# Optimization experiments

Hardware: AMD Instinct MI355X
Metric: run time of the kernel (lower is better)

The kernel has to match this reference:

```python
import jax, jax.numpy as jnp
import numpy as np

B, N, C_IN = 8, 2048, 2


def _pdist(x):
    # (B,N,N) pairwise euclidean distances
    d2 = jnp.sum((x[:, :, None, :] - x[:, None, :, :]) ** 2, axis=-1)
    return jnp.sqrt(d2)


def _knn_idx(x, k):
    d = _pdist(x)
    return jnp.argsort(d, axis=-1)[:, :, :k]  # includes self (dist 0)


def _ball_idx(x, radius, nsample):
    # deterministic ball query: neighbors with dist<=radius in ascending index
    # order, cyclically repeated if fewer than nsample (self is always in ball)
    d = _pdist(x)
    n = x.shape[1]
    mask = d <= radius
    ar = jnp.arange(n)
    order = jnp.argsort(jnp.where(mask, ar, ar + n), axis=-1)  # valid idx first
    count = jnp.sum(mask, axis=-1, keepdims=True)               # >= 1
    pos = jnp.arange(nsample)[None, None, :] % count            # (B,N,nsample)
    return jnp.take_along_axis(order, pos, axis=-1)


def _gather(x, idx):
    # x: (B,N,C), idx: (B,N,S) -> (B,N,S,C)
    return jax.vmap(lambda pts, ind: pts[ind])(x, idx)


def _mlp2(f, w0, b0, w1, b1):
    # 1x1 Conv2D stack == per-neighbor dense + relu
    f = jnp.maximum(jnp.einsum('bnsc,cd->bnsd', f, w0) + b0, 0.0)
    f = jnp.maximum(jnp.einsum('bnsc,cd->bnsd', f, w1) + b1, 0.0)
    return f


def _dense_relu(x, w, b):
    return jnp.maximum(x @ w + b, 0.0)


def _forward(x,
             sa1_w0, sa1_b0, sa1_w1, sa1_b1,
             sa2_w0, sa2_b0, sa2_w1, sa2_b1,
             sa3_w0, sa3_b0, sa3_w1, sa3_b1,
             fp1_w0, fp1_b0, fp1_w1, fp1_b1,
             fp2_w0, fp2_b0, fp2_w1, fp2_b1,
             fc1_w, fc1_b, fc2_w, fc2_b, out_w, out_b):
    # SA1: knn(k=32) on raw points, mlps [64,64], mean over neighbors
    x1 = jnp.mean(_mlp2(_gather(x, _knn_idx(x, 32)), sa1_w0, sa1_b0, sa1_w1, sa1_b1), axis=2)
    # SA2: ball query radius=0.2, nsample=32, mlps [128,128]
    x2 = jnp.mean(_mlp2(_gather(x1, _ball_idx(x1, 0.2, 32)), sa2_w0, sa2_b0, sa2_w1, sa2_b1), axis=2)
    # SA3: ball query radius=0.4, nsample=64, mlps [256,256]
    x3 = jnp.mean(_mlp2(_gather(x2, _ball_idx(x2, 0.4, 64)), sa3_w0, sa3_b0, sa3_w1, sa3_b1), axis=2)
    # FP1: dense mlps on local (x2), concat global (x3)
    h = _dense_relu(_dense_relu(x2, fp1_w0, fp1_b0), fp1_w1, fp1_b1)
    h = jnp.concatenate([h, x3], axis=-1)
    # FP2: dense mlps on local (x1), concat previous
    g = _dense_relu(_dense_relu(x1, fp2_w0, fp2_b0), fp2_w1, fp2_b1)
    g = jnp.concatenate([g, h], axis=-1)
    g = _dense_relu(g, fc1_w, fc1_b)
    g = _dense_relu(g, fc2_w, fc2_b)
    return jax.nn.sigmoid(g @ out_w + out_b)  # (B,N,1)


def setup_inputs() -> dict:
    key = jax.random.key(0)
    ks = iter(jax.random.split(key, 40))
    def w(i, o):
        return (jax.random.normal(next(ks), (i, o), jnp.float32) / np.sqrt(i)).astype(jnp.float32)
    def b(o):
        return jnp.zeros((o,), jnp.float32)
    inp = {
        'x': jax.random.normal(next(ks), (B, N, C_IN), jnp.float32),
        'sa1_w0': w(2, 64),   'sa1_b0': b(64),  'sa1_w1': w(64, 64),   'sa1_b1': b(64),
        'sa2_w0': w(64, 128), 'sa2_b0': b(128), 'sa2_w1': w(128, 128), 'sa2_b1': b(128),
        'sa3_w0': w(128, 256),'sa3_b0': b(256), 'sa3_w1': w(256, 256), 'sa3_b1': b(256),
        'fp1_w0': w(128, 512),'fp1_b0': b(512), 'fp1_w1': w(512, 512), 'fp1_b1': b(512),
        'fp2_w0': w(64, 256), 'fp2_b0': b(256), 'fp2_w1': w(256, 256), 'fp2_b1': b(256),
        'fc1_w': w(1024, 256),'fc1_b': b(256),
        'fc2_w': w(256, 128), 'fc2_b': b(128),
        'out_w': w(128, 1),   'out_b': b(1),
    }
    return inp


def reference(x,
              sa1_w0, sa1_b0, sa1_w1, sa1_b1,
              sa2_w0, sa2_b0, sa2_w1, sa2_b1,
              sa3_w0, sa3_b0, sa3_w1, sa3_b1,
              fp1_w0, fp1_b0, fp1_w1, fp1_b1,
              fp2_w0, fp2_b0, fp2_w1, fp2_b1,
              fc1_w, fc1_b, fc2_w, fc2_b, out_w, out_b):
    return _forward(x,
                    sa1_w0, sa1_b0, sa1_w1, sa1_b1,
                    sa2_w0, sa2_b0, sa2_w1, sa2_b1,
                    sa3_w0, sa3_b0, sa3_w1, sa3_b1,
                    fp1_w0, fp1_b0, fp1_w1, fp1_b1,
                    fp2_w0, fp2_b0, fp2_w1, fp2_b1,
                    fc1_w, fc1_b, fc2_w, fc2_b, out_w, out_b)
```

## Files before the change

kernel.cpp:

```cpp
#include <hip/hip_runtime.h>
#include <hip/hip_bf16.h>
#include <cstdint>

#define M_ROWS 16384

typedef __attribute__((ext_vector_type(8))) short short8;
typedef __attribute__((ext_vector_type(4))) float f32x4;

__device__ __forceinline__ unsigned long long umin64(unsigned long long a,
                                                     unsigned long long b) {
  return a < b ? a : b;
}

struct TJobs {
  const float* W[8];
  __hip_bfloat16* Wt[8];
  int K[8], N[8], bx[8], off[8];
};

__global__ __launch_bounds__(256) void prologue_kernel(
    TJobs jb, int toff,
    const float* __restrict__ x,
    const float* __restrict__ w0,
    const float* __restrict__ b0,
    const float* __restrict__ w1,
    const float* __restrict__ b1,
    float* __restrict__ G1)
{
  __shared__ float tile[32][33];
  __shared__ __align__(16) float Ts[64][68];
  __shared__ __align__(16) float Ws[64][68];
  __shared__ float xs[64][2];
  __shared__ float w0s[2][64];
  __shared__ float b0s[64];
  int bid = blockIdx.x;
  int tid = threadIdx.x;
  if (bid < toff) {
    int j = 0;
#pragma unroll
    for (int t = 1; t < 8; t++)
      if (bid >= jb.off[t]) j = t;
    int rel = bid - jb.off[j];
    int K = jb.K[j], N = jb.N[j];
    const float* W = jb.W[j];
    __hip_bfloat16* Wt = jb.Wt[j];
    int n0 = (rel % jb.bx[j]) << 5, k0 = (rel / jb.bx[j]) << 5;
    int c = tid & 31, i0 = tid >> 5;
#pragma unroll
    for (int p = 0; p < 4; p++) {
      int i = i0 + p * 8;
      tile[i][c] = W[(size_t)(k0 + i) * N + n0 + c];
    }
    __syncthreads();
#pragma unroll
    for (int p = 0; p < 4; p++) {
      int r = i0 + p * 8;
      Wt[(size_t)(n0 + r) * K + k0 + c] = (__hip_bfloat16)tile[c][r];
    }
    return;
  }
  int m0 = (bid - toff) << 6;
  if (tid < 128) {
    ((float*)xs)[tid] = x[(size_t)m0 * 2 + tid];
  } else if (tid < 192) {
    int n = tid - 128;
    w0s[0][n] = w0[n];
    b0s[n] = b0[n];
  } else {
    int n = tid - 192;
    w0s[1][n] = w0[64 + n];
  }
#pragma unroll
  for (int i = 0; i < 16; i++) {
    int idx = tid + (i << 8);
    int k = idx >> 6, n = idx & 63;
    Ws[k][n] = w1[(size_t)k * 64 + n];
  }
  __syncthreads();
#pragma unroll
  for (int i = 0; i < 16; i++) {
    int idx = tid + (i << 8);
    int m = idx >> 6, n = idx & 63;
    float acc = 0.f;
    acc += xs[m][0] * w0s[0][n];
    acc += xs[m][1] * w0s[1][n];
    Ts[n][m] = fmaxf(acc + b0s[n], 0.f);
  }
  __syncthreads();
  int tx = tid & 15, ty = tid >> 4;
  float acc[4][4] = {};
  for (int k = 0; k < 64; k++) {
    float4 a4 = *(const float4*)&Ts[k][ty << 2];
    float4 b4 = *(const float4*)&Ws[k][tx << 2];
    float av[4] = {a4.x, a4.y, a4.z, a4.w};
    float bv[4] = {b4.x, b4.y, b4.z, b4.w};
#pragma unroll
    for (int i = 0; i < 4; i++)
#pragma unroll
      for (int j = 0; j < 4; j++)
        acc[i][j] += av[i] * bv[j];
  }
  float4 bb = *(const float4*)&b1[tx << 2];
  float bv[4] = {bb.x, bb.y, bb.z, bb.w};
#pragma unroll
  for (int i = 0; i < 4; i++) {
    int m = m0 + (ty << 2) + i;
    float4 o;
    o.x = fmaxf(acc[i][0] + bv[0], 0.f);
    o.y = fmaxf(acc[i][1] + bv[1], 0.f);
    o.z = fmaxf(acc[i][2] + bv[2], 0.f);
    o.w = fmaxf(acc[i][3] + bv[3], 0.f);
    *(float4*)&G1[(size_t)m * 64 + (tx << 2)] = o;
  }
}

__global__ __launch_bounds__(256) void sa2_fused(
    const float* __restrict__ X1,
    const float* __restrict__ w0,
    const float* __restrict__ b0,
    const float* __restrict__ w1,
    const float* __restrict__ b1,
    float* __restrict__ H2)
{
  __shared__ __align__(16) float Ts[128][68];
  __shared__ __align__(16) float Bs[16][132];
  __shared__ __align__(16) float Xs[16][68];
  int tid = threadIdx.x;
  int tx = tid & 15, ty = tid >> 4;
  int m0 = blockIdx.x << 6;
  float acc1[4][8] = {};
  for (int k0 = 0; k0 < 64; k0 += 16) {
#pragma unroll
    for (int i = 0; i < 4; i++) {
      int idx = tid + (i << 8);
      int m = idx >> 4, k = idx & 15;
      Xs[k][m] = X1[(size_t)(m0 + m) * 64 + k0 + k];
    }
#pragma unroll
    for (int i = 0; i < 8; i++) {
      int idx = tid + (i << 8);
      int n = idx & 127, k = idx >> 7;
      Bs[k][n] = w0[(size_t)(k0 + k) * 128 + n];
    }
    __syncthreads();
#pragma unroll
    for (int k = 0; k < 16; k++) {
      float av[4], bv[8];
#pragma unroll
      for (int i = 0; i < 4; i++) av[i] = Xs[k][ty * 4 + i];
#pragma unroll
      for (int j = 0; j < 8; j++) bv[j] = Bs[k][tx * 8 + j];
#pragma unroll
      for (int i = 0; i < 4; i++)
#pragma unroll
        for (int j = 0; j < 8; j++)
          acc1[i][j] += av[i] * bv[j];
    }
    __syncthreads();
  }
#pragma unroll
  for (int j = 0; j < 8; j++) {
    float bbv = b0[tx * 8 + j];
#pragma unroll
    for (int i = 0; i < 4; i++)
      Ts[tx * 8 + j][ty * 4 + i] = fmaxf(acc1[i][j] + bbv, 0.f);
  }
  __syncthreads();
  float acc2[4][8] = {};
  for (int k0 = 0; k0 < 128; k0 += 16) {
#pragma unroll
    for (int i = 0; i < 8; i++) {
      int idx = tid + (i << 8);
      int n = idx & 127, k = idx >> 7;
      Bs[k][n] = w1[(size_t)(k0 + k) * 128 + n];
    }
    __syncthreads();
#pragma unroll
    for (int k = 0; k < 16; k++) {
      float av[4], bv[8];
#pragma unroll
      for (int i = 0; i < 4; i++) av[i] = Ts[k0 + k][ty * 4 + i];
#pragma unroll
      for (int j = 0; j < 8; j++) bv[j] = Bs[k][tx * 8 + j];
#pragma unroll
      for (int i = 0; i < 4; i++)
#pragma unroll
        for (int j = 0; j < 8; j++)
          acc2[i][j] += av[i] * bv[j];
    }
    __syncthreads();
  }
#pragma unroll
  for (int i = 0; i < 4; i++) {
    int m = m0 + ty * 4 + i;
#pragma unroll
    for (int j = 0; j < 8; j++) {
      int n = tx * 8 + j;
      H2[(size_t)m * 128 + n] = fmaxf(acc2[i][j] + b1[n], 0.f);
    }
  }
}

template <bool OUT_BF16>
__global__ __launch_bounds__(256) void gemm_mfma(
    const __hip_bfloat16* __restrict__ A, int lda,
    const __hip_bfloat16* __restrict__ Wt, int ldw,
    const float* __restrict__ bias,
    void* __restrict__ Y, int ldy, int N, int K)
{
  __shared__ __align__(16) short As[128][40];
  __shared__ __align__(16) short Bs[128][40];
  int tid = threadIdx.x;
  int wave = tid >> 6, lane = tid & 63;
  int quad = lane >> 4, l16 = lane & 15;
  int m0 = blockIdx.y << 7, n0 = blockIdx.x << 7;
  int wm = (wave >> 1) << 6, wn = (wave & 1) << 6;
  f32x4 acc[4][4] = {};
  const short* Ag = (const short*)A;
  const short* Bg = (const short*)Wt;
  int srow = tid >> 2, sq = tid & 3;
  for (int k0 = 0; k0 < K; k0 += 32) {
#pragma unroll
    for (int h = 0; h < 2; h++) {
      int r = srow + (h << 6);
      uint4 va = *(const uint4*)&Ag[(size_t)(m0 + r) * lda + k0 + sq * 8];
      *(uint4*)&As[r][sq * 8] = va;
      uint4 vb = *(const uint4*)&Bg[(size_t)(n0 + r) * ldw + k0 + sq * 8];
      *(uint4*)&Bs[r][sq * 8] = vb;
    }
    __syncthreads();
    short8 a[4], b[4];
#pragma unroll
    for (int mi = 0; mi < 4; mi++)
      a[mi] = *(const short8*)&As[wm + mi * 16 + l16][quad * 8];
#pragma unroll
    for (int ni = 0; ni < 4; ni++)
      b[ni] = *(const short8*)&Bs[wn + ni * 16 + l16][quad * 8];
#pragma unroll
    for (int mi = 0; mi < 4; mi++)
#pragma unroll
      for (int ni = 0; ni < 4; ni++)
        acc[mi][ni] = __builtin_amdgcn_mfma_f32_16x16x32_bf16(
            a[mi], b[ni], acc[mi][ni], 0, 0, 0);
    __syncthreads();
  }
  float bn[4];
#pragma unroll
  for (int ni = 0; ni < 4; ni++) bn[ni] = bias[n0 + wn + ni * 16 + l16];
#pragma unroll
  for (int mi = 0; mi < 4; mi++)
#pragma unroll
    for (int ni = 0; ni < 4; ni++) {
      int n = n0 + wn + ni * 16 + l16;
#pragma unroll
      for (int r = 0; r < 4; r++) {
        int m = m0 + wm + mi * 16 + quad * 4 + r;
        float v = fmaxf(acc[mi][ni][r] + bn[ni], 0.f);
        if (OUT_BF16)
          ((__hip_bfloat16*)Y)[(size_t)m * ldy + n] = (__hip_bfloat16)v;
        else
          ((float*)Y)[(size_t)m * ldy + n] = v;
      }
    }
}

struct GJobs {
  const short* A[3];
  const short* W[3];
  const float* bias[3];
  __hip_bfloat16* Y[3];
  int lda[3], ldw[3], ldy[3], N[3], K[3], xt[3], off[3];
};

__global__ __launch_bounds__(256) void gemm_mfma_multi(GJobs g)
{
  __shared__ __align__(16) short As[128][40];
  __shared__ __align__(16) short Bs[128][40];
  int bid = blockIdx.x;
  int j = 0;
#pragma unroll
  for (int t = 1; t < 3; t++)
    if (bid >= g.off[t]) j = t;
  int rel = bid - g.off[j];
  int xt = g.xt[j];
  int m0 = (rel / xt) << 7, n0 = (rel % xt) << 7;
  int lda = g.lda[j], ldw = g.ldw[j], ldy = g.ldy[j], K = g.K[j];
  const short* Ag = g.A[j];
  const short* Bg = g.W[j];
  const float* bias = g.bias[j];
  __hip_bfloat16* Y = g.Y[j];

  int tid = threadIdx.x;
  int wave = tid >> 6, lane = tid & 63;
  int quad = lane >> 4, l16 = lane & 15;
  int wm = (wave >> 1) << 6, wn = (wave & 1) << 6;
  f32x4 acc[4][4] = {};
  int srow = tid >> 2, sq = tid & 3;
  for (int k0 = 0; k0 < K; k0 += 32) {
#pragma unroll
    for (int h = 0; h < 2; h++) {
      int r = srow + (h << 6);
      uint4 va = *(const uint4*)&Ag[(size_t)(m0 + r) * lda + k0 + sq * 8];
      *(uint4*)&As[r][sq * 8] = va;
      uint4 vb = *(const uint4*)&Bg[(size_t)(n0 + r) * ldw + k0 + sq * 8];
      *(uint4*)&Bs[r][sq * 8] = vb;
    }
    __syncthreads();
    short8 a[4], b[4];
#pragma unroll
    for (int mi = 0; mi < 4; mi++)
      a[mi] = *(const short8*)&As[wm + mi * 16 + l16][quad * 8];
#pragma unroll
    for (int ni = 0; ni < 4; ni++)
      b[ni] = *(const short8*)&Bs[wn + ni * 16 + l16][quad * 8];
#pragma unroll
    for (int mi = 0; mi < 4; mi++)
#pragma unroll
      for (int ni = 0; ni < 4; ni++)
        acc[mi][ni] = __builtin_amdgcn_mfma_f32_16x16x32_bf16(
            a[mi], b[ni], acc[mi][ni], 0, 0, 0);
    __syncthreads();
  }
  float bn[4];
#pragma unroll
  for (int ni = 0; ni < 4; ni++) bn[ni] = bias[n0 + wn + ni * 16 + l16];
#pragma unroll
  for (int mi = 0; mi < 4; mi++)
#pragma unroll
    for (int ni = 0; ni < 4; ni++) {
      int n = n0 + wn + ni * 16 + l16;
#pragma unroll
      for (int r = 0; r < 4; r++) {
        int m = m0 + wm + mi * 16 + quad * 4 + r;
        float v = fmaxf(acc[mi][ni][r] + bn[ni], 0.f);
        Y[(size_t)m * ldy + n] = (__hip_bfloat16)v;
      }
    }
}

__global__ __launch_bounds__(256) void gemm_fc2_out(
    const __hip_bfloat16* __restrict__ A,
    const __hip_bfloat16* __restrict__ Wt,
    const float* __restrict__ bias,
    const float* __restrict__ wout,
    const float* __restrict__ bout,
    float* __restrict__ out)
{
  __shared__ __align__(16) short As[128][40];
  __shared__ __align__(16) short Bs[128][40];
  __shared__ float red[128][2];
  const int N = 128, K = 256, lda = 256, ldw = 256;
  int tid = threadIdx.x;
  int wave = tid >> 6, lane = tid & 63;
  int quad = lane >> 4, l16 = lane & 15;
  int m0 = blockIdx.y << 7;
  int wm = (wave >> 1) << 6, wn = (wave & 1) << 6;
  f32x4 acc[4][4] = {};
  const short* Ag = (const short*)A;
  const short* Bg = (const short*)Wt;
  int srow = tid >> 2, sq = tid & 3;
  for (int k0 = 0; k0 < K; k0 += 32) {
#pragma unroll
    for (int h = 0; h < 2; h++) {
      int r = srow + (h << 6);
      uint4 va = *(const uint4*)&Ag[(size_t)(m0 + r) * lda + k0 + sq * 8];
      *(uint4*)&As[r][sq * 8] = va;
      uint4 vb = *(const uint4*)&Bg[(size_t)(r % N) * ldw + k0 + sq * 8];
      *(uint4*)&Bs[r][sq * 8] = vb;
    }
    __syncthreads();
    short8 a[4], b[4];
#pragma unroll
    for (int mi = 0; mi < 4; mi++)
      a[mi] = *(const short8*)&As[wm + mi * 16 + l16][quad * 8];
#pragma unroll
    for (int ni = 0; ni < 4; ni++)
      b[ni] = *(const short8*)&Bs[wn + ni * 16 + l16][quad * 8];
#pragma unroll
    for (int mi = 0; mi < 4; mi++)
#pragma unroll
      for (int ni = 0; ni < 4; ni++)
        acc[mi][ni] = __builtin_amdgcn_mfma_f32_16x16x32_bf16(
            a[mi], b[ni], acc[mi][ni], 0, 0, 0);
    __syncthreads();
  }
  float bn[4], wo[4];
#pragma unroll
  for (int ni = 0; ni < 4; ni++) {
    int n = wn + ni * 16 + l16;
    bn[ni] = bias[n];
    wo[ni] = wout[n];
  }
  float sacc[4][4];
#pragma unroll
  for (int mi = 0; mi < 4; mi++)
#pragma unroll
    for (int r = 0; r < 4; r++) {
      float s = 0.f;
#pragma unroll
      for (int ni = 0; ni < 4; ni++)
        s += fmaxf(acc[mi][ni][r] + bn[ni], 0.f) * wo[ni];
      sacc[mi][r] = s;
    }
#pragma unroll
  for (int off = 1; off < 16; off <<= 1)
#pragma unroll
    for (int mi = 0; mi < 4; mi++)
#pragma unroll
      for (int r = 0; r < 4; r++)
        sacc[mi][r] += __shfl_xor(sacc[mi][r], off);
  int wp = wave & 1;
  if (l16 == 0) {
#pragma unroll
    for (int mi = 0; mi < 4; mi++)
#pragma unroll
      for (int r = 0; r < 4; r++)
        red[wm + mi * 16 + quad * 4 + r][wp] = sacc[mi][r];
  }
  __syncthreads();
  if (tid < 128) {
    float s = red[tid][0] + red[tid][1] + bout[0];
    out[(size_t)(m0 + tid)] = 1.f / (1.f + expf(-s));
  }
}

__global__ __launch_bounds__(256) void knn_mean4(
    const float* __restrict__ X,
    const float* __restrict__ G1,
    float* __restrict__ X1,
    __hip_bfloat16* __restrict__ X1b,
    __hip_bfloat16* __restrict__ X1lo,
    float* __restrict__ nrmX1)
{
  int blk = blockIdx.x;
  int qb = ((blk & 7) << 11) + ((blk >> 3) << 2);
  int base = qb & ~2047;
  int tid = threadIdx.x;
  int wave = tid >> 6, lane = tid & 63;
  __shared__ unsigned long long lmins[4][256];
  __shared__ unsigned long long qmins[4][64];
  __shared__ unsigned long long thr[4];
  __shared__ unsigned long long surv[4][256];
  __shared__ int scnt[4];
  __shared__ int selidx[4][32];
  if (tid < 4) scnt[tid] = 0;
  float xj[8], yj[8];
#pragma unroll
  for (int u = 0; u < 8; u++) {
    int j = (u << 8) + tid;
    float2 c = *(const float2*)&X[(size_t)(base + j) * 2];
    xj[u] = c.x;
    yj[u] = c.y;
  }
  unsigned long long key[4][8];
#pragma unroll
  for (int g = 0; g < 4; g++) {
    float qx = X[(size_t)(qb + g) * 2];
    float qy = X[(size_t)(qb + g) * 2 + 1];
    unsigned long long lm = ~0ull;
#pragma unroll
    for (int u = 0; u < 8; u++) {
      float dx = xj[u] - qx;
      float dy = yj[u] - qy;
      float d2 = dx * dx + dy * dy;
      key[g][u] = ((unsigned long long)__float_as_uint(d2) << 32) |
                  (unsigned)((u << 8) + tid);
      lm = umin64(lm, key[g][u]);
    }
    lmins[g][tid] = lm;
  }
  __syncthreads();
  {
    int g = wave;
    unsigned long long qm =
        umin64(umin64(lmins[g][lane], lmins[g][lane + 64]),
               umin64(lmins[g][lane + 128], lmins[g][lane + 192]));
    qmins[g][lane] = qm;
    int rank = 0;
    for (int i = 0; i < 64; i++) rank += (qmins[g][i] < qm);
    if (rank == 31) thr[g] = qm;
  }
  __syncthreads();
#pragma unroll
  for (int g = 0; g < 4; g++) {
    unsigned long long T = thr[g];
#pragma unroll
    for (int u = 0; u < 8; u++) {
      if (key[g][u] <= T) {
        int p = atomicAdd(&scnt[g], 1);
        if (p < 256) surv[g][p] = key[g][u];
      }
    }
  }
  __syncthreads();
  int ovf[4] = {scnt[0], scnt[1], scnt[2], scnt[3]};
  {
    int g = wave;
    int s = ovf[g];
    if (s <= 256) {
      for (int i = lane; i < s; i += 64) {
        unsigned long long c = surv[g][i];
        int r = 0;
        for (int j2 = 0; j2 < s; j2++) r += (surv[g][j2] < c);
        if (r < 32) selidx[g][r] = (int)(c & 0xffffffffULL);
      }
    }
  }
  if (ovf[0] > 256 || ovf[1] > 256 || ovf[2] > 256 || ovf[3] > 256) {
    unsigned long long* ob = &lmins[0][0];
    for (int g = 0; g < 4; g++) {
      if (ovf[g] <= 256) continue;
      __syncthreads();
      if (tid == 0) scnt[g] = 0;
      __syncthreads();
      unsigned long long T = thr[g];
#pragma unroll
      for (int u = 0; u < 8; u++) {
        if (key[g][u] <= T) {
          int p = atomicAdd(&scnt[g], 1);
          ob[p] = key[g][u];
        }
      }
      __syncthreads();
      int s2 = scnt[g];
      for (int i = tid; i < s2; i += 256) {
        unsigned long long c = ob[i];
        int r = 0;
        for (int j2 = 0; j2 < s2; j2++) r += (ob[j2] < c);
        if (r < 32) selidx[g][r] = (int)(c & 0xffffffffULL);
      }
    }
    __syncthreads();
  }
  {
    int g = wave;
    float acc = 0.f;
#pragma unroll 8
    for (int sI = 0; sI < 32; sI++)
      acc += G1[(size_t)(base + selidx[g][sI]) * 64 + lane];
    float v = acc * (1.0f / 32.0f);
    int q = qb + g;
    X1[(size_t)q * 64 + lane] = v;
    __hip_bfloat16 hi = (__hip_bfloat16)v;
    X1b[(size_t)q * 64 + lane] = hi;
    X1lo[(size_t)q * 64 + lane] = (__hip_bfloat16)(v - (float)hi);
    float nv = v * v;
#pragma unroll
    for (int off = 32; off > 0; off >>= 1) nv += __shfl_down(nv, off);
    if (lane == 0) nrmX1[q] = nv;
  }
}

template <int C>
__global__ __launch_bounds__(256) void ball_mask_mfma(
    const float* __restrict__ F32,
    const __hip_bfloat16* __restrict__ Fhi,
    const __hip_bfloat16* __restrict__ Flo,
    const float* __restrict__ nrm,
    unsigned long long* __restrict__ mask,
    float r2)
{
  __shared__ __align__(16) short Qh[128][40];
  __shared__ __align__(16) short Ql[128][40];
  __shared__ __align__(16) short Ch[128][40];
  __shared__ __align__(16) short Cl[128][40];
  __shared__ unsigned int tw[128][4];
  __shared__ float nqs[128], ncs[128];
  int tid = threadIdx.x;
  int p = blockIdx.x;
  int qt = 0;
  while (p >= 16 - qt) { p -= 16 - qt; qt++; }
  int ct = qt + p;
  int b0 = blockIdx.y << 11;
  int q0 = b0 + (qt << 7), c0 = b0 + (ct << 7);
  tw[tid >> 1][(tid & 1) * 2] = 0;
  tw[tid >> 1][(tid & 1) * 2 + 1] = 0;
  if (tid < 128) nqs[tid] = nrm[q0 + tid];
  else ncs[tid - 128] = nrm[c0 + tid - 128];

  int wave = tid >> 6, lane = tid & 63;
  int quad = lane >> 4, l16 = lane & 15;
  int wm = (wave >> 1) << 6, wn = (wave & 1) << 6;
  f32x4 acc[4][4] = {};
  const short* QH = (const short*)Fhi;
  const short* QL = (const short*)Flo;
  int srow = tid >> 2, sq = tid & 3;
  for (int k0 = 0; k0 < C; k0 += 32) {
#pragma unroll
    for (int h = 0; h < 2; h++) {
      int r = srow + (h << 6);
      *(uint4*)&Qh[r][sq * 8] = *(const uint4*)&QH[(size_t)(q0 + r) * C + k0 + sq * 8];
      *(uint4*)&Ql[r][sq * 8] = *(const uint4*)&QL[(size_t)(q0 + r) * C + k0 + sq * 8];
      *(uint4*)&Ch[r][sq * 8] = *(const uint4*)&QH[(size_t)(c0 + r) * C + k0 + sq * 8];
      *(uint4*)&Cl[r][sq * 8] = *(const uint4*)&QL[(size_t)(c0 + r) * C + k0 + sq * 8];
    }
    __syncthreads();
    short8 ah[4], al[4];
#pragma unroll
    for (int mi = 0; mi < 4; mi++) {
      ah[mi] = *(const short8*)&Qh[wm + mi * 16 + l16][quad * 8];
      al[mi] = *(const short8*)&Ql[wm + mi * 16 + l16][quad * 8];
    }
#pragma unroll
    for (int ni = 0; ni < 4; ni++) {
      short8 bh = *(const short8*)&Ch[wn + ni * 16 + l16][quad * 8];
      short8 bl = *(const short8*)&Cl[wn + ni * 16 + l16][quad * 8];
#pragma unroll
      for (int mi = 0; mi < 4; mi++) {
        acc[mi][ni] = __builtin_amdgcn_mfma_f32_16x16x32_bf16(ah[mi], bh, acc[mi][ni], 0, 0, 0);
        acc[mi][ni] = __builtin_amdgcn_mfma_f32_16x16x32_bf16(ah[mi], bl, acc[mi][ni], 0, 0, 0);
        acc[mi][ni] = __builtin_amdgcn_mfma_f32_16x16x32_bf16(al[mi], bh, acc[mi][ni], 0, 0, 0);
      }
    }
    __syncthreads();
  }
  unsigned long long memb = 0, fb = 0;
#pragma unroll
  for (int mi = 0; mi < 4; mi++)
#pragma unroll
    for (int ni = 0; ni < 4; ni++)
#pragma unroll
      for (int r = 0; r < 4; r++) {
        int e = (mi << 4) | (ni << 2) | r;
        float nqv = nqs[wm + mi * 16 + quad * 4 + r];
        float ncv = ncs[wn + ni * 16 + l16];
        float d2a = nqv + ncv - 2.f * acc[mi][ni][r];
        float eps = 4.0e-5f * (nqv + ncv) + 1.0e-6f;
        if (d2a < r2 - eps) memb |= 1ull << e;
        else if (d2a <= r2 + eps) fb |= 1ull << e;
      }
  while (fb) {
    int e = __builtin_ctzll(fb);
    fb &= fb - 1;
    int mi = e >> 4, ni = (e >> 2) & 3, r = e & 3;
    int qrow = q0 + wm + mi * 16 + quad * 4 + r;
    int ccol = c0 + wn + ni * 16 + l16;
    float a2 = 0.f;
    for (int k = 0; k < C; k++) {
      float d = F32[(size_t)qrow * C + k] - F32[(size_t)ccol * C + k];
      a2 = fmaf(d, d, a2);
    }
    if (a2 <= r2) memb |= 1ull << e;
  }
#pragma unroll
  for (int ni = 0; ni < 4; ni++) {
    int cl = wn + ni * 16 + l16;
    unsigned int w0b = 0, w1b = 0;
#pragma unroll
    for (int mi = 0; mi < 4; mi++)
#pragma unroll
      for (int r = 0; r < 4; r++)
        if (memb & (1ull << ((mi << 4) | (ni << 2) | r))) {
          unsigned int bitpos = ((mi & 1) << 4) | (quad << 2) | r;
          if (mi < 2) w0b |= 1u << bitpos;
          else w1b |= 1u << bitpos;
        }
    if (w0b) atomicOr(&tw[cl][(wm >> 5)], w0b);
    if (w1b) atomicOr(&tw[cl][(wm >> 5) + 1], w1b);
  }
  __syncthreads();
  {
    int row = tid >> 1, half = tid & 1;
    int wq = row >> 5, sb = row & 31;
    unsigned int lo = 0, hi = 0;
    for (int j = 0; j < 32; j++) {
      lo |= ((tw[half * 64 + j][wq] >> sb) & 1u) << j;
      hi |= ((tw[half * 64 + 32 + j][wq] >> sb) & 1u) << j;
    }
    mask[(size_t)(q0 + row) * 32 + (ct << 1) + half] =
        ((unsigned long long)hi << 32) | lo;
  }
  if (qt != ct) {
    int row = tid >> 1, word = tid & 1;
    unsigned long long v = (unsigned long long)tw[row][word * 2] |
                           ((unsigned long long)tw[row][word * 2 + 1] << 32);
    mask[(size_t)(c0 + row) * 32 + (qt << 1) + word] = v;
  }
}

__global__ __launch_bounds__(256) void ball_gather4_f32(
    const unsigned long long* __restrict__ mask,
    const float* __restrict__ H, int CH,
    float* __restrict__ Yf, __hip_bfloat16* __restrict__ Yb,
    __hip_bfloat16* __restrict__ Ylo, float* __restrict__ nrm,
    int ldy, int S)
{
  int blk = blockIdx.x;
  int tid = threadIdx.x;
  int wave = tid >> 6, lane = tid & 63;
  int q = ((blk & 7) << 11) + ((blk >> 3) << 2) + wave;
  int base = q & ~2047;
  __shared__ int idxl[4][64];
  __shared__ float wtab[4][64];
  __shared__ int scount[4];
  if (lane < 32) {
    unsigned long long w = mask[(size_t)q * 32 + lane];
    int cnt = __popcll(w);
    int inc = cnt;
#pragma unroll
    for (int off = 1; off < 32; off <<= 1) {
      int o = __shfl_up(inc, off);
      if (lane >= off) inc += o;
    }
    if (lane == 31) scount[wave] = inc;
    int p = inc - cnt;
    while (w && p < 64) {
      int j = (lane << 6) + __builtin_ctzll(w);
      w &= w - 1;
      idxl[wave][p++] = j;
    }
  }
  int c = scount[wave];
  {
    int p = lane;
    int cnt = (p < c && p < S) ? ((S - 1 - p) / c + 1) : 0;
    wtab[wave][p] = (float)cnt / (float)S;
  }
  float acc0 = 0.f, acc1 = 0.f;
  int lim = c < S ? c : S;
#pragma unroll 4
  for (int s = 0; s < lim; s++) {
    float wv = wtab[wave][s];
    float2 v = *(const float2*)&H[(size_t)(base + idxl[wave][s]) * CH + lane * 2];
    acc0 += wv * v.x;
    acc1 += wv * v.y;
  }
  int n0 = lane * 2;
  if (Yf) *(float2*)&Yf[(size_t)q * ldy + n0] = make_float2(acc0, acc1);
  if (Yb) {
    Yb[(size_t)q * ldy + n0] = (__hip_bfloat16)acc0;
    Yb[(size_t)q * ldy + n0 + 1] = (__hip_bfloat16)acc1;
  }
  if (Ylo) {
    __hip_bfloat16 h0 = (__hip_bfloat16)acc0, h1 = (__hip_bfloat16)acc1;
    Ylo[(size_t)q * ldy + n0] = (__hip_bfloat16)(acc0 - (float)h0);
    Ylo[(size_t)q * ldy + n0 + 1] = (__hip_bfloat16)(acc1 - (float)h1);
  }
  if (nrm) {
    float nv = acc0 * acc0 + acc1 * acc1;
#pragma unroll
    for (int off = 32; off > 0; off >>= 1) nv += __shfl_down(nv, off);
    if (lane == 0) nrm[q] = nv;
  }
}

__global__ __launch_bounds__(256) void ball_gather4_bf16(
    const unsigned long long* __restrict__ mask,
    const __hip_bfloat16* __restrict__ H, int CH,
    __hip_bfloat16* __restrict__ Yb, int ldy, int S)
{
  int blk = blockIdx.x;
  int tid = threadIdx.x;
  int wave = tid >> 6, lane = tid & 63;
  int q = ((blk & 7) << 11) + ((blk >> 3) << 2) + wave;
  int base = q & ~2047;
  __shared__ int idxl[4][64];
  __shared__ float wtab[4][64];
  __shared__ int scount[4];
  if (lane < 32) {
    unsigned long long w = mask[(size_t)q * 32 + lane];
    int cnt = __popcll(w);
    int inc = cnt;
#pragma unroll
    for (int off = 1; off < 32; off <<= 1) {
      int o = __shfl_up(inc, off);
      if (lane >= off) inc += o;
    }
    if (lane == 31) scount[wave] = inc;
    int p = inc - cnt;
    while (w && p < 64) {
      int j = (lane << 6) + __builtin_ctzll(w);
      w &= w - 1;
      idxl[wave][p++] = j;
    }
  }
  int c = scount[wave];
  {
    int p = lane;
    int cnt = (p < c && p < S) ? ((S - 1 - p) / c + 1) : 0;
    wtab[wave][p] = (float)cnt / (float)S;
  }
  const unsigned short* Hs = (const unsigned short*)H;
  float acc[4] = {0.f, 0.f, 0.f, 0.f};
  int lim = c < S ? c : S;
#pragma unroll 4
  for (int s = 0; s < lim; s++) {
    float wv = wtab[wave][s];
    uint2 v = *(const uint2*)&Hs[(size_t)(base + idxl[wave][s]) * CH + lane * 4];
    acc[0] += wv * __uint_as_float(v.x << 16);
    acc[1] += wv * __uint_as_float(v.x & 0xffff0000u);
    acc[2] += wv * __uint_as_float(v.y << 16);
    acc[3] += wv * __uint_as_float(v.y & 0xffff0000u);
  }
  int n0 = lane * 4;
#pragma unroll
  for (int j = 0; j < 4; j++)
    Yb[(size_t)q * ldy + n0 + j] = (__hip_bfloat16)acc[j];
}

extern "C" void kernel_launch(void* const* d_in, const int* in_sizes, int n_in,
                              void* d_out, int out_size, void* d_ws,
                              size_t ws_size, hipStream_t stream)
{
  const float* x      = (const float*)d_in[0];
  const float* sa1_w0 = (const float*)d_in[1];
  const float* sa1_b0 = (const float*)d_in[2];
  const float* sa1_w1 = (const float*)d_in[3];
  const float* sa1_b1 = (const float*)d_in[4];
  const float* sa2_w0 = (const float*)d_in[5];
  const float* sa2_b0 = (const float*)d_in[6];
  const float* sa2_w1 = (const float*)d_in[7];
  const float* sa2_b1 = (const float*)d_in[8];
  const float* sa3_w0 = (const float*)d_in[9];
  const float* sa3_b0 = (const float*)d_in[10];
  const float* sa3_w1 = (const float*)d_in[11];
  const float* sa3_b1 = (const float*)d_in[12];
  const float* fp1_w0 = (const float*)d_in[13];
  const float* fp1_b0 = (const float*)d_in[14];
  const float* fp1_w1 = (const float*)d_in[15];
  const float* fp1_b1 = (const float*)d_in[16];
  const float* fp2_w0 = (const float*)d_in[17];
  const float* fp2_b0 = (const float*)d_in[18];
  const float* fp2_w1 = (const float*)d_in[19];
  const float* fp2_b1 = (const float*)d_in[20];
  const float* fc1_w  = (const float*)d_in[21];
  const float* fc1_b  = (const float*)d_in[22];
  const float* fc2_w  = (const float*)d_in[23];
  const float* fc2_b  = (const float*)d_in[24];
  const float* out_w  = (const float*)d_in[25];
  const float* out_b  = (const float*)d_in[26];
  float* out = (float*)d_out;

  const size_t M = M_ROWS;
  float* ws = (float*)d_ws;
  float* G1  = ws + M * 256;
  float* X1  = ws + M * 320;
  float* X2  = ws + M * 384;
  float* H2  = ws + M * 512;
  __hip_bfloat16* H3b16 = (__hip_bfloat16*)(ws + M * 640);
  unsigned long long* MASK = (unsigned long long*)(ws + M * 896);
  __hip_bfloat16* X1b = (__hip_bfloat16*)(ws + M * 960);
  __hip_bfloat16* X2b = (__hip_bfloat16*)(ws + M * 992);
  __hip_bfloat16* TB0 = (__hip_bfloat16*)(ws + M * 1056);
  __hip_bfloat16* TB1 = (__hip_bfloat16*)(ws + M * 1184);
  __hip_bfloat16* TB2 = (__hip_bfloat16*)(ws + M * 1440);
  __hip_bfloat16* G   = (__hip_bfloat16*)(ws + M * 1568);
  __hip_bfloat16* H3b = (__hip_bfloat16*)(ws + M * 2080);
  __hip_bfloat16* WB  = (__hip_bfloat16*)(ws + M * 2208);
  __hip_bfloat16* X1lo = (__hip_bfloat16*)(ws + M * 2240);
  __hip_bfloat16* X2lo = (__hip_bfloat16*)(ws + M * 2272);
  float* nrmX1 = ws + M * 2336;
  float* nrmX2 = ws + M * 2337;
  if (ws_size < (size_t)M * 2340 * sizeof(float)) return;
  __hip_bfloat16* w_sa3_0 = WB;
  __hip_bfloat16* w_sa3_1 = w_sa3_0 + 32768;
  __hip_bfloat16* w_fp1_0 = w_sa3_1 + 65536;
  __hip_bfloat16* w_fp1_1 = w_fp1_0 + 65536;
  __hip_bfloat16* w_fp2_0 = w_fp1_1 + 262144;
  __hip_bfloat16* w_fp2_1 = w_fp2_0 + 16384;
  __hip_bfloat16* w_fc1   = w_fp2_1 + 65536;
  __hip_bfloat16* w_fc2   = w_fc1 + 262144;

  dim3 blk(256);
  TJobs jb;
  const float* srcs[8] = {sa3_w0, sa3_w1, fp1_w0, fp1_w1, fp2_w0, fp2_w1, fc1_w, fc2_w};
  __hip_bfloat16* dsts[8] = {w_sa3_0, w_sa3_1, w_fp1_0, w_fp1_1, w_fp2_0, w_fp2_1, w_fc1, w_fc2};
  int Ks[8] = {128, 256, 128, 512, 64, 256, 1024, 256};
  int Ns[8] = {256, 256, 512, 512, 256, 256, 256, 128};
  int off = 0;
  for (int i = 0; i < 8; i++) {
    jb.W[i] = srcs[i]; jb.Wt[i] = dsts[i];
    jb.K[i] = Ks[i]; jb.N[i] = Ns[i];
    jb.bx[i] = Ns[i] >> 5;
    jb.off[i] = off;
    off += (Ns[i] >> 5) * (Ks[i] >> 5);
  }
  prologue_kernel<<<off + 256, blk, 0, stream>>>(jb, off, x, sa1_w0, sa1_b0,
                                                 sa1_w1, sa1_b1, G1);
  knn_mean4<<<4096, 256, 0, stream>>>(x, G1, X1, X1b, X1lo, nrmX1);
  sa2_fused<<<256, blk, 0, stream>>>(X1, sa2_w0, sa2_b0, sa2_w1, sa2_b1, H2);
  ball_mask_mfma<64><<<dim3(136, 8), blk, 0, stream>>>(X1, X1b, X1lo, nrmX1, MASK, 0.2f * 0.2f);
  ball_gather4_f32<<<4096, blk, 0, stream>>>(MASK, H2, 128, X2, X2b, X2lo, nrmX2, 128, 32);
  ball_mask_mfma<128><<<dim3(136, 8), blk, 0, stream>>>(X2, X2b, X2lo, nrmX2, MASK, 0.4f * 0.4f);
  {
    GJobs g1;
    g1.A[0] = (const short*)X2b; g1.W[0] = (const short*)w_sa3_0; g1.bias[0] = sa3_b0;
    g1.Y[0] = TB0; g1.lda[0] = 128; g1.ldw[0] = 128; g1.ldy[0] = 256; g1.N[0] = 256; g1.K[0] = 128;
    g1.A[1] = (const short*)X2b; g1.W[1] = (const short*)w_fp1_0; g1.bias[1] = fp1_b0;
    g1.Y[1] = TB1; g1.lda[1] = 128; g1.ldw[1] = 128; g1.ldy[1] = 512; g1.N[1] = 512; g1.K[1] = 128;
    g1.A[2] = (const short*)X1b; g1.W[2] = (const short*)w_fp2_0; g1.bias[2] = fp2_b0;
    g1.Y[2] = TB2; g1.lda[2] = 64; g1.ldw[2] = 64; g1.ldy[2] = 256; g1.N[2] = 256; g1.K[2] = 64;
    int tot1 = 0;
    for (int i = 0; i < 3; i++) {
      g1.xt[i] = g1.N[i] >> 7;
      g1.off[i] = tot1;
      tot1 += g1.xt[i] * 128;
    }
    gemm_mfma_multi<<<tot1, blk, 0, stream>>>(g1);

    GJobs g2;
    g2.A[0] = (const short*)TB0; g2.W[0] = (const short*)w_sa3_1; g2.bias[0] = sa3_b1;
    g2.Y[0] = H3b16; g2.lda[0] = 256; g2.ldw[0] = 256; g2.ldy[0] = 256; g2.N[0] = 256; g2.K[0] = 256;
    g2.A[1] = (const short*)TB1; g2.W[1] = (const short*)w_fp1_1; g2.bias[1] = fp1_b1;
    g2.Y[1] = G + 256; g2.lda[1] = 512; g2.ldw[1] = 512; g2.ldy[1] = 1024; g2.N[1] = 512; g2.K[1] = 512;
    g2.A[2] = (const short*)TB2; g2.W[2] = (const short*)w_fp2_1; g2.bias[2] = fp2_b1;
    g2.Y[2] = G; g2.lda[2] = 256; g2.ldw[2] = 256; g2.ldy[2] = 1024; g2.N[2] = 256; g2.K[2] = 256;
    int tot2 = 0;
    for (int i = 0; i < 3; i++) {
      g2.xt[i] = g2.N[i] >> 7;
      g2.off[i] = tot2;
      tot2 += g2.xt[i] * 128;
    }
    gemm_mfma_multi<<<tot2, blk, 0, stream>>>(g2);
  }
  ball_gather4_bf16<<<4096, blk, 0, stream>>>(MASK, H3b16, 256, G + 768, 1024, 64);
  gemm_mfma<true><<<dim3(2, 128), blk, 0, stream>>>(G, 1024, w_fc1, 1024, fc1_b, H3b, 256, 256, 1024);
  gemm_fc2_out<<<dim3(1, 128), blk, 0, stream>>>(H3b, w_fc2, fc2_b, out_w, out_b, out);
}
```

Measured before the change: 340.2 us.

## Merge independent kernels into shared launches via block-index dispatch

Refactors the SA2 MLP, ball mask and MFMA GEMM into device bodies that run on a shared-memory buffer, so independent stages can share one launch. SA2 runs alongside the radius-0.2 ball mask in one grid. The FP1/FP2 second-layer GEMMs run alongside the SA3 ball gather in a fused tail kernel, and the SA3 second GEMM is split out to run before it. This cuts launch gaps and lets independent work fill the GPU, at the cost of a larger shared-memory footprint per block, which may lower occupancy, and one extra launch for the split GEMM.

```diff
diff --git a/kernel.cpp b/kernel.cpp
--- a/kernel.cpp
+++ b/kernel.cpp
@@ -114,20 +114,19 @@
   }
 }
 
-__global__ __launch_bounds__(256) void sa2_fused(
+__device__ void sa2_body(char* smem,
     const float* __restrict__ X1,
     const float* __restrict__ w0,
     const float* __restrict__ b0,
     const float* __restrict__ w1,
     const float* __restrict__ b1,
-    float* __restrict__ H2)
-{
-  __shared__ __align__(16) float Ts[128][68];
-  __shared__ __align__(16) float Bs[16][132];
-  __shared__ __align__(16) float Xs[16][68];
+    float* __restrict__ H2, int m0)
+{
+  float (*Ts)[68] = (float(*)[68])smem;
+  float (*Bs)[132] = (float(*)[132])(smem + 34816);
+  float (*Xs)[68] = (float(*)[68])(smem + 43264);
   int tid = threadIdx.x;
   int tx = tid & 15, ty = tid >> 4;
-  int m0 = blockIdx.x << 6;
   float acc1[4][8] = {};
   for (int k0 = 0; k0 < 64; k0 += 16) {
 #pragma unroll
@@ -201,377 +200,28 @@
   }
 }
 
-template <bool OUT_BF16>
-__global__ __launch_bounds__(256) void gemm_mfma(
-    const __hip_bfloat16* __restrict__ A, int lda,
-    const __hip_bfloat16* __restrict__ Wt, int ldw,
-    const float* __restrict__ bias,
-    void* __restrict__ Y, int ldy, int N, int K)
-{
-  __shared__ __align__(16) short As[128][40];
-  __shared__ __align__(16) short Bs[128][40];
-  int tid = threadIdx.x;
-  int wave = tid >> 6, lane = tid & 63;
-  int quad = lane >> 4, l16 = lane & 15;
-  int m0 = blockIdx.y << 7, n0 = blockIdx.x << 7;
-  int wm = (wave >> 1) << 6, wn = (wave & 1) << 6;
-  f32x4 acc[4][4] = {};
-  const short* Ag = (const short*)A;
-  const short* Bg = (const short*)Wt;
-  int srow = tid >> 2, sq = tid & 3;
-  for (int k0 = 0; k0 < K; k0 += 32) {
-#pragma unroll
-    for (int h = 0; h < 2; h++) {
-      int r = srow + (h << 6);
-      uint4 va = *(const uint4*)&Ag[(size_t)(m0 + r) * lda + k0 + sq * 8];
-      *(uint4*)&As[r][sq * 8] = va;
-      uint4 vb = *(const uint4*)&Bg[(size_t)(n0 + r) * ldw + k0 + sq * 8];
-      *(uint4*)&Bs[r][sq * 8] = vb;
-    }
-    __syncthreads();
-    short8 a[4], b[4];
-#pragma unroll
-    for (int mi = 0; mi < 4; mi++)
-      a[mi] = *(const short8*)&As[wm + mi * 16 + l16][quad * 8];
-#pragma unroll
-    for (int ni = 0; ni < 4; ni++)
-      b[ni] = *(const short8*)&Bs[wn + ni * 16 + l16][quad * 8];
-#pragma unroll
-    for (int mi = 0; mi < 4; mi++)
-#pragma unroll
-      for (int ni = 0; ni < 4; ni++)
-        acc[mi][ni] = __builtin_amdgcn_mfma_f32_16x16x32_bf16(
-            a[mi], b[ni], acc[mi][ni], 0, 0, 0);
-    __syncthreads();
-  }
-  float bn[4];
-#pragma unroll
-  for (int ni = 0; ni < 4; ni++) bn[ni] = bias[n0 + wn + ni * 16 + l16];
-#pragma unroll
-  for (int mi = 0; mi < 4; mi++)
-#pragma unroll
-    for (int ni = 0; ni < 4; ni++) {
-      int n = n0 + wn + ni * 16 + l16;
-#pragma unroll
-      for (int r = 0; r < 4; r++) {
-        int m = m0 + wm + mi * 16 + quad * 4 + r;
-        float v = fmaxf(acc[mi][ni][r] + bn[ni], 0.f);
-        if (OUT_BF16)
-          ((__hip_bfloat16*)Y)[(size_t)m * ldy + n] = (__hip_bfloat16)v;
-        else
-          ((float*)Y)[(size_t)m * ldy + n] = v;
-      }
-    }
-}
-
-struct GJobs {
-  const short* A[3];
-  const short* W[3];
-  const float* bias[3];
-  __hip_bfloat16* Y[3];
-  int lda[3], ldw[3], ldy[3], N[3], K[3], xt[3], off[3];
-};
-
-__global__ __launch_bounds__(256) void gemm_mfma_multi(GJobs g)
-{
-  __shared__ __align__(16) short As[128][40];
-  __shared__ __align__(16) short Bs[128][40];
-  int bid = blockIdx.x;
-  int j = 0;
-#pragma unroll
-  for (int t = 1; t < 3; t++)
-    if (bid >= g.off[t]) j = t;
-  int rel = bid - g.off[j];
-  int xt = g.xt[j];
-  int m0 = (rel / xt) << 7, n0 = (rel % xt) << 7;
-  int lda = g.lda[j], ldw = g.ldw[j], ldy = g.ldy[j], K = g.K[j];
-  const short* Ag = g.A[j];
-  const short* Bg = g.W[j];
-  const float* bias = g.bias[j];
-  __hip_bfloat16* Y = g.Y[j];
-
-  int tid = threadIdx.x;
-  int wave = tid >> 6, lane = tid & 63;
-  int quad = lane >> 4, l16 = lane & 15;
-  int wm = (wave >> 1) << 6, wn = (wave & 1) << 6;
-  f32x4 acc[4][4] = {};
-  int srow = tid >> 2, sq = tid & 3;
-  for (int k0 = 0; k0 < K; k0 += 32) {
-#pragma unroll
-    for (int h = 0; h < 2; h++) {
-      int r = srow + (h << 6);
-      uint4 va = *(const uint4*)&Ag[(size_t)(m0 + r) * lda + k0 + sq * 8];
-      *(uint4*)&As[r][sq * 8] = va;
-      uint4 vb = *(const uint4*)&Bg[(size_t)(n0 + r) * ldw + k0 + sq * 8];
-      *(uint4*)&Bs[r][sq * 8] = vb;
-    }
-    __syncthreads();
-    short8 a[4], b[4];
-#pragma unroll
-    for (int mi = 0; mi < 4; mi++)
-      a[mi] = *(const short8*)&As[wm + mi * 16 + l16][quad * 8];
-#pragma unroll
-    for (int ni = 0; ni < 4; ni++)
-      b[ni] = *(const short8*)&Bs[wn + ni * 16 + l16][quad * 8];
-#pragma unroll
-    for (int mi = 0; mi < 4; mi++)
-#pragma unroll
-      for (int ni = 0; ni < 4; ni++)
-        acc[mi][ni] = __builtin_amdgcn_mfma_f32_16x16x32_bf16(
-            a[mi], b[ni], acc[mi][ni], 0, 0, 0);
-    __syncthreads();
-  }
-  float bn[4];
-#pragma unroll
-  for (int ni = 0; ni < 4; ni++) bn[ni] = bias[n0 + wn + ni * 16 + l16];
-#pragma unroll
-  for (int mi = 0; mi < 4; mi++)
-#pragma unroll
-    for (int ni = 0; ni < 4; ni++) {
-      int n = n0 + wn + ni * 16 + l16;
-#pragma unroll
-      for (int r = 0; r < 4; r++) {
-        int m = m0 + wm + mi * 16 + quad * 4 + r;
-        float v = fmaxf(acc[mi][ni][r] + bn[ni], 0.f);
-        Y[(size_t)m * ldy + n] = (__hip_bfloat16)v;
-      }
-    }
-}
-
-__global__ __launch_bounds__(256) void gemm_fc2_out(
-    const __hip_bfloat16* __restrict__ A,
-    const __hip_bfloat16* __restrict__ Wt,
-    const float* __restrict__ bias,
-    const float* __restrict__ wout,
-    const float* __restrict__ bout,
-    float* __restrict__ out)
-{
-  __shared__ __align__(16) short As[128][40];
-  __shared__ __align__(16) short Bs[128][40];
-  __shared__ float red[128][2];
-  const int N = 128, K = 256, lda = 256, ldw = 256;
-  int tid = threadIdx.x;
-  int wave = tid >> 6, lane = tid & 63;
-  int quad = lane >> 4, l16 = lane & 15;
-  int m0 = blockIdx.y << 7;
-  int wm = (wave >> 1) << 6, wn = (wave & 1) << 6;
-  f32x4 acc[4][4] = {};
-  const short* Ag = (const short*)A;
-  const short* Bg = (const short*)Wt;
-  int srow = tid >> 2, sq = tid & 3;
-  for (int k0 = 0; k0 < K; k0 += 32) {
-#pragma unroll
-    for (int h = 0; h < 2; h++) {
-      int r = srow + (h << 6);
-      uint4 va = *(const uint4*)&Ag[(size_t)(m0 + r) * lda + k0 + sq * 8];
-      *(uint4*)&As[r][sq * 8] = va;
-      uint4 vb = *(const uint4*)&Bg[(size_t)(r % N) * ldw + k0 + sq * 8];
-      *(uint4*)&Bs[r][sq * 8] = vb;
-    }
-    __syncthreads();
-    short8 a[4], b[4];
-#pragma unroll
-    for (int mi = 0; mi < 4; mi++)
-      a[mi] = *(const short8*)&As[wm + mi * 16 + l16][quad * 8];
-#pragma unroll
-    for (int ni = 0; ni < 4; ni++)
-      b[ni] = *(const short8*)&Bs[wn + ni * 16 + l16][quad * 8];
-#pragma unroll
-    for (int mi = 0; mi < 4; mi++)
-#pragma unroll
-      for (int ni = 0; ni < 4; ni++)
-        acc[mi][ni] = __builtin_amdgcn_mfma_f32_16x16x32_bf16(
-            a[mi], b[ni], acc[mi][ni], 0, 0, 0);
-    __syncthreads();
-  }
-  float bn[4], wo[4];
-#pragma unroll
-  for (int ni = 0; ni < 4; ni++) {
-    int n = wn + ni * 16 + l16;
-    bn[ni] = bias[n];
-    wo[ni] = wout[n];
-  }
-  float sacc[4][4];
-#pragma unroll
-  for (int mi = 0; mi < 4; mi++)
-#pragma unroll
-    for (int r = 0; r < 4; r++) {
-      float s = 0.f;
-#pragma unroll
-      for (int ni = 0; ni < 4; ni++)
-        s += fmaxf(acc[mi][ni][r] + bn[ni], 0.f) * wo[ni];
-      sacc[mi][r] = s;
-    }
-#pragma unroll
-  for (int off = 1; off < 16; off <<= 1)
-#pragma unroll
-    for (int mi = 0; mi < 4; mi++)
-#pragma unroll
-      for (int r = 0; r < 4; r++)
-        sacc[mi][r] += __shfl_xor(sacc[mi][r], off);
-  int wp = wave & 1;
-  if (l16 == 0) {
-#pragma unroll
-    for (int mi = 0; mi < 4; mi++)
-#pragma unroll
-      for (int r = 0; r < 4; r++)
-        red[wm + mi * 16 + quad * 4 + r][wp] = sacc[mi][r];
-  }
-  __syncthreads();
-  if (tid < 128) {
-    float s = red[tid][0] + red[tid][1] + bout[0];
-    out[(size_t)(m0 + tid)] = 1.f / (1.f + expf(-s));
-  }
-}
-
-__global__ __launch_bounds__(256) void knn_mean4(
-    const float* __restrict__ X,
-    const float* __restrict__ G1,
-    float* __restrict__ X1,
-    __hip_bfloat16* __restrict__ X1b,
-    __hip_bfloat16* __restrict__ X1lo,
-    float* __restrict__ nrmX1)
-{
-  int blk = blockIdx.x;
-  int qb = ((blk & 7) << 11) + ((blk >> 3) << 2);
-  int base = qb & ~2047;
-  int tid = threadIdx.x;
-  int wave = tid >> 6, lane = tid & 63;
-  __shared__ unsigned long long lmins[4][256];
-  __shared__ unsigned long long qmins[4][64];
-  __shared__ unsigned long long thr[4];
-  __shared__ unsigned long long surv[4][256];
-  __shared__ int scnt[4];
-  __shared__ int selidx[4][32];
-  if (tid < 4) scnt[tid] = 0;
-  float xj[8], yj[8];
-#pragma unroll
-  for (int u = 0; u < 8; u++) {
-    int j = (u << 8) + tid;
-    float2 c = *(const float2*)&X[(size_t)(base + j) * 2];
-    xj[u] = c.x;
-    yj[u] = c.y;
-  }
-  unsigned long long key[4][8];
-#pragma unroll
-  for (int g = 0; g < 4; g++) {
-    float qx = X[(size_t)(qb + g) * 2];
-    float qy = X[(size_t)(qb + g) * 2 + 1];
-    unsigned long long lm = ~0ull;
-#pragma unroll
-    for (int u = 0; u < 8; u++) {
-      float dx = xj[u] - qx;
-      float dy = yj[u] - qy;
-      float d2 = dx * dx + dy * dy;
-      key[g][u] = ((unsigned long long)__float_as_uint(d2) << 32) |
-                  (unsigned)((u << 8) + tid);
-      lm = umin64(lm, key[g][u]);
-    }
-    lmins[g][tid] = lm;
-  }
-  __syncthreads();
-  {
-    int g = wave;
-    unsigned long long qm =
-        umin64(umin64(lmins[g][lane], lmins[g][lane + 64]),
-               umin64(lmins[g][lane + 128], lmins[g][lane + 192]));
-    qmins[g][lane] = qm;
-    int rank = 0;
-    for (int i = 0; i < 64; i++) rank += (qmins[g][i] < qm);
-    if (rank == 31) thr[g] = qm;
-  }
-  __syncthreads();
-#pragma unroll
-  for (int g = 0; g < 4; g++) {
-    unsigned long long T = thr[g];
-#pragma unroll
-    for (int u = 0; u < 8; u++) {
-      if (key[g][u] <= T) {
-        int p = atomicAdd(&scnt[g], 1);
-        if (p < 256) surv[g][p] = key[g][u];
-      }
-    }
-  }
-  __syncthreads();
-  int ovf[4] = {scnt[0], scnt[1], scnt[2], scnt[3]};
-  {
-    int g = wave;
-    int s = ovf[g];
-    if (s <= 256) {
-      for (int i = lane; i < s; i += 64) {
-        unsigned long long c = surv[g][i];
-        int r = 0;
-        for (int j2 = 0; j2 < s; j2++) r += (surv[g][j2] < c);
-        if (r < 32) selidx[g][r] = (int)(c & 0xffffffffULL);
-      }
-    }
-  }
-  if (ovf[0] > 256 || ovf[1] > 256 || ovf[2] > 256 || ovf[3] > 256) {
-    unsigned long long* ob = &lmins[0][0];
-    for (int g = 0; g < 4; g++) {
-      if (ovf[g] <= 256) continue;
-      __syncthreads();
-      if (tid == 0) scnt[g] = 0;
-      __syncthreads();
-      unsigned long long T = thr[g];
-#pragma unroll
-      for (int u = 0; u < 8; u++) {
-        if (key[g][u] <= T) {
-          int p = atomicAdd(&scnt[g], 1);
-          ob[p] = key[g][u];
-        }
-      }
-      __syncthreads();
-      int s2 = scnt[g];
-      for (int i = tid; i < s2; i += 256) {
-        unsigned long long c = ob[i];
-        int r = 0;
-        for (int j2 = 0; j2 < s2; j2++) r += (ob[j2] < c);
-        if (r < 32) selidx[g][r] = (int)(c & 0xffffffffULL);
-      }
-    }
-    __syncthreads();
-  }
-  {
-    int g = wave;
-    float acc = 0.f;
-#pragma unroll 8
-    for (int sI = 0; sI < 32; sI++)
-      acc += G1[(size_t)(base + selidx[g][sI]) * 64 + lane];
-    float v = acc * (1.0f / 32.0f);
-    int q = qb + g;
-    X1[(size_t)q * 64 + lane] = v;
-    __hip_bfloat16 hi = (__hip_bfloat16)v;
-    X1b[(size_t)q * 64 + lane] = hi;
-    X1lo[(size_t)q * 64 + lane] = (__hip_bfloat16)(v - (float)hi);
-    float nv = v * v;
-#pragma unroll
-    for (int off = 32; off > 0; off >>= 1) nv += __shfl_down(nv, off);
-    if (lane == 0) nrmX1[q] = nv;
-  }
-}
-
 template <int C>
-__global__ __launch_bounds__(256) void ball_mask_mfma(
+__device__ void ball_body(char* smem,
     const float* __restrict__ F32,
     const __hip_bfloat16* __restrict__ Fhi,
     const __hip_bfloat16* __restrict__ Flo,
     const float* __restrict__ nrm,
     unsigned long long* __restrict__ mask,
-    float r2)
-{
-  __shared__ __align__(16) short Qh[128][40];
-  __shared__ __align__(16) short Ql[128][40];
-  __shared__ __align__(16) short Ch[128][40];
-  __shared__ __align__(16) short Cl[128][40];
-  __shared__ unsigned int tw[128][4];
-  __shared__ float nqs[128], ncs[128];
+    float r2, int pairIdx, int batch)
+{
+  short (*Qh)[40] = (short(*)[40])smem;
+  short (*Ql)[40] = (short(*)[40])(smem + 10240);
+  short (*Ch)[40] = (short(*)[40])(smem + 20480);
+  short (*Cl)[40] = (short(*)[40])(smem + 30720);
+  unsigned int (*tw)[4] = (unsigned int(*)[4])(smem + 40960);
+  float* nqs = (float*)(smem + 43008);
+  float* ncs = (float*)(smem + 43520);
   int tid = threadIdx.x;
-  int p = blockIdx.x;
+  int p = pairIdx;
   int qt = 0;
   while (p >= 16 - qt) { p -= 16 - qt; qt++; }
   int ct = qt + p;
-  int b0 = blockIdx.y << 11;
+  int b0 = batch << 11;
   int q0 = b0 + (qt << 7), c0 = b0 + (ct << 7);
   tw[tid >> 1][(tid & 1) * 2] = 0;
   tw[tid >> 1][(tid & 1) * 2 + 1] = 0;
@@ -678,6 +328,205 @@
   }
 }
 
+__global__ __launch_bounds__(256) void fused_sa2_ball64(
+    const float* __restrict__ X1,
+    const __hip_bfloat16* __restrict__ X1b,
+    const __hip_bfloat16* __restrict__ X1lo,
+    const float* __restrict__ nrmX1,
+    unsigned long long* __restrict__ MASK, float r2,
+    const float* __restrict__ w0, const float* __restrict__ b0,
+    const float* __restrict__ w1, const float* __restrict__ b1,
+    float* __restrict__ H2)
+{
+  __shared__ __align__(16) char smem[47616];
+  int bid = blockIdx.x;
+  if (bid < 1088)
+    ball_body<64>(smem, X1, X1b, X1lo, nrmX1, MASK, r2, bid % 136, bid / 136);
+  else
+    sa2_body(smem, X1, w0, b0, w1, b1, H2, (bid - 1088) << 6);
+}
+
+template <int C>
+__global__ __launch_bounds__(256) void ball_mask_mfma(
+    const float* __restrict__ F32,
+    const __hip_bfloat16* __restrict__ Fhi,
+    const __hip_bfloat16* __restrict__ Flo,
+    const float* __restrict__ nrm,
+    unsigned long long* __restrict__ mask,
+    float r2)
+{
+  __shared__ __align__(16) char smem[44032];
+  ball_body<C>(smem, F32, Fhi, Flo, nrm, mask, r2, blockIdx.x, blockIdx.y);
+}
+
+__device__ void mfma_body(char* smem,
+    const short* __restrict__ Ag, const short* __restrict__ Bg,
+    const float* __restrict__ bias, __hip_bfloat16* __restrict__ Y,
+    int lda, int ldw, int ldy, int K, int m0, int n0)
+{
+  short (*As)[40] = (short(*)[40])smem;
+  short (*Bs)[40] = (short(*)[40])(smem + 10240);
+  int tid = threadIdx.x;
+  int wave = tid >> 6, lane = tid & 63;
+  int quad = lane >> 4, l16 = lane & 15;
+  int wm = (wave >> 1) << 6, wn = (wave & 1) << 6;
+  f32x4 acc[4][4] = {};
+  int srow = tid >> 2, sq = tid & 3;
+  for (int k0 = 0; k0 < K; k0 += 32) {
+#pragma unroll
+    for (int h = 0; h < 2; h++) {
+      int r = srow + (h << 6);
+      uint4 va = *(const uint4*)&Ag[(size_t)(m0 + r) * lda + k0 + sq * 8];
+      *(uint4*)&As[r][sq * 8] = va;
+      uint4 vb = *(const uint4*)&Bg[(size_t)(n0 + r) * ldw + k0 + sq * 8];
+      *(uint4*)&Bs[r][sq * 8] = vb;
+    }
+    __syncthreads();
+    short8 a[4], b[4];
+#pragma unroll
+    for (int mi = 0; mi < 4; mi++)
+      a[mi] = *(const short8*)&As[wm + mi * 16 + l16][quad * 8];
+#pragma unroll
+    for (int ni = 0; ni < 4; ni++)
+      b[ni] = *(const short8*)&Bs[wn + ni * 16 + l16][quad * 8];
+#pragma unroll
+    for (int mi = 0; mi < 4; mi++)
+#pragma unroll
+      for (int ni = 0; ni < 4; ni++)
+        acc[mi][ni] = __builtin_amdgcn_mfma_f32_16x16x32_bf16(
+            a[mi], b[ni], acc[mi][ni], 0, 0, 0);
+    __syncthreads();
+  }
+  float bn[4];
+#pragma unroll
+  for (int ni = 0; ni < 4; ni++) bn[ni] = bias[n0 + wn + ni * 16 + l16];
+#pragma unroll
+  for (int mi = 0; mi < 4; mi++)
+#pragma unroll
+    for (int ni = 0; ni < 4; ni++) {
+      int n = n0 + wn + ni * 16 + l16;
+#pragma unroll
+      for (int r = 0; r < 4; r++) {
+        int m = m0 + wm + mi * 16 + quad * 4 + r;
+        float v = fmaxf(acc[mi][ni][r] + bn[ni], 0.f);
+        Y[(size_t)m * ldy + n] = (__hip_bfloat16)v;
+      }
+    }
+}
+
+__global__ __launch_bounds__(256) void gemm_mfma_bf16(
+    const __hip_bfloat16* __restrict__ A, int lda,
+    const __hip_bfloat16* __restrict__ Wt, int ldw,
+    const float* __restrict__ bias,
+    __hip_bfloat16* __restrict__ Y, int ldy, int K)
+{
+  __shared__ __align__(16) char smem[20480];
+  mfma_body(smem, (const short*)A, (const short*)Wt, bias, Y,
+            lda, ldw, ldy, K, blockIdx.y << 7, blockIdx.x << 7);
+}
+
+struct GJobs {
+  const short* A[3];
+  const short* W[3];
+  const float* bias[3];
+  __hip_bfloat16* Y[3];
+  int lda[3], ldw[3], ldy[3], N[3], K[3], xt[3], off[3];
+};
+
+__global__ __launch_bounds__(256) void gemm_mfma_multi(GJobs g)
+{
+  __shared__ __align__(16) char smem[20480];
+  int bid = blockIdx.x;
+  int j = 0;
+#pragma unroll
+  for (int t = 1; t < 3; t++)
+    if (bid >= g.off[t]) j = t;
+  int rel = bid - g.off[j];
+  mfma_body(smem, g.A[j], g.W[j], g.bias[j], g.Y[j],
+            g.lda[j], g.ldw[j], g.ldy[j], g.K[j],
+            (rel / g.xt[j]) << 7, (rel % g.xt[j]) << 7);
+}
+
+__device__ void gather_bf16_body(char* smem, int blk,
+    const unsigned long long* __restrict__ mask,
+    const __hip_bfloat16* __restrict__ H, int CH,
+    __hip_bfloat16* __restrict__ Yb, int ldy, int S)
+{
+  int (*idxl)[64] = (int(*)[64])smem;
+  float (*wtab)[64] = (float(*)[64])(smem + 1024);
+  int* scount = (int*)(smem + 2048);
+  int tid = threadIdx.x;
+  int wave = tid >> 6, lane = tid & 63;
+  int q = ((blk & 7) << 11) + ((blk >> 3) << 2) + wave;
+  int base = q & ~2047;
+  if (lane < 32) {
+    unsigned long long w = mask[(size_t)q * 32 + lane];
+    int cnt = __popcll(w);
+    int inc = cnt;
+#pragma unroll
+    for (int off = 1; off < 32; off <<= 1) {
+      int o = __shfl_up(inc, off);
+      if (lane >= off) inc += o;
+    }
+    if (lane == 31) scount[wave] = inc;
+    int p = inc - cnt;
+    while (w && p < 64) {
+      int j = (lane << 6) + __builtin_ctzll(w);
+      w &= w - 1;
+      idxl[wave][p++] = j;
+    }
+  }
+  int c = scount[wave];
+  {
+    int p = lane;
+    int cnt = (p < c && p < S) ? ((S - 1 - p) / c + 1) : 0;
+    wtab[wave][p] = (float)cnt / (float)S;
+  }
+  const unsigned short* Hs = (const unsigned short*)H;
+  float acc[4] = {0.f, 0.f, 0.f, 0.f};
+  int lim = c < S ? c : S;
+#pragma unroll 4
+  for (int s = 0; s < lim; s++) {
+    float wv = wtab[wave][s];
+    uint2 v = *(const uint2*)&Hs[(size_t)(base + idxl[wave][s]) * CH + lane * 4];
+    acc[0] += wv * __uint_as_float(v.x << 16);
+    acc[1] += wv * __uint_as_float(v.x & 0xffff0000u);
+    acc[2] += wv * __uint_as_float(v.y << 16);
+    acc[3] += wv * __uint_as_float(v.y & 0xffff0000u);
+  }
+  int n0 = lane * 4;
+#pragma unroll
+  for (int j = 0; j < 4; j++)
+    Yb[(size_t)q * ldy + n0 + j] = (__hip_bfloat16)acc[j];
+}
+
+struct GJobs2 {
+  const short* A[2];
+  const short* W[2];
+  const float* bias[2];
+  __hip_bfloat16* Y[2];
+  int lda[2], ldw[2], ldy[2], K[2], xt[2], off[2];
+};
+
+__global__ __launch_bounds__(256) void fused_tail(
+    GJobs2 g, int goff,
+    const unsigned long long* __restrict__ mask,
+    const __hip_bfloat16* __restrict__ H, int CH,
+    __hip_bfloat16* __restrict__ Yb, int ldy, int S)
+{
+  __shared__ __align__(16) char smem[20480];
+  int bid = blockIdx.x;
+  if (bid < goff) {
+    int j = (bid >= g.off[1]) ? 1 : 0;
+    int rel = bid - g.off[j];
+    mfma_body(smem, g.A[j], g.W[j], g.bias[j], g.Y[j],
+              g.lda[j], g.ldw[j], g.ldy[j], g.K[j],
+              (rel / g.xt[j]) << 7, (rel % g.xt[j]) << 7);
+    return;
+  }
+  gather_bf16_body(smem, bid - goff, mask, H, CH, Yb, ldy, S);
+}
+
 __global__ __launch_bounds__(256) void ball_gather4_f32(
     const unsigned long long* __restrict__ mask,
     const float* __restrict__ H, int CH,
@@ -744,58 +593,217 @@
   }
 }
 
-__global__ __launch_bounds__(256) void ball_gather4_bf16(
-    const unsigned long long* __restrict__ mask,
-    const __hip_bfloat16* __restrict__ H, int CH,
-    __hip_bfloat16* __restrict__ Yb, int ldy, int S)
-{
-  int blk = blockIdx.x;
+__global__ __launch_bounds__(256) void gemm_fc2_out(
+    const __hip_bfloat16* __restrict__ A,
+    const __hip_bfloat16* __restrict__ Wt,
+    const float* __restrict__ bias,
+    const float* __restrict__ wout,
+    const float* __restrict__ bout,
+    float* __restrict__ out)
+{
+  __shared__ __align__(16) short As[128][40];
+  __shared__ __align__(16) short Bs[128][40];
+  __shared__ float red[128][2];
+  const int N = 128, K = 256, lda = 256, ldw = 256;
   int tid = threadIdx.x;
   int wave = tid >> 6, lane = tid & 63;
-  int q = ((blk & 7) << 11) + ((blk >> 3) << 2) + wave;
-  int base = q & ~2047;
-  __shared__ int idxl[4][64];
-  __shared__ float wtab[4][64];
-  __shared__ int scount[4];
-  if (lane < 32) {
-    unsigned long long w = mask[(size_t)q * 32 + lane];
-    int cnt = __popcll(w);
-    int inc = cnt;
-#pragma unroll
-    for (int off = 1; off < 32; off <<= 1) {
-      int o = __shfl_up(inc, off);
-      if (lane >= off) inc += o;
-    }
-    if (lane == 31) scount[wave] = inc;
-    int p = inc - cnt;
-    while (w && p < 64) {
-      int j = (lane << 6) + __builtin_ctzll(w);
-      w &= w - 1;
-      idxl[wave][p++] = j;
-    }
-  }
-  int c = scount[wave];
+  int quad = lane >> 4, l16 = lane & 15;
+  int m0 = blockIdx.y << 7;
+  int wm = (wave >> 1) << 6, wn = (wave & 1) << 6;
+  f32x4 acc[4][4] = {};
+  const short* Ag = (const short*)A;
+  const short* Bg = (const short*)Wt;
+  int srow = tid >> 2, sq = tid & 3;
+  for (int k0 = 0; k0 < K; k0 += 32) {
+#pragma unroll
+    for (int h = 0; h < 2; h++) {
+      int r = srow + (h << 6);
+      uint4 va = *(const uint4*)&Ag[(size_t)(m0 + r) * lda + k0 + sq * 8];
+      *(uint4*)&As[r][sq * 8] = va;
+      uint4 vb = *(const uint4*)&Bg[(size_t)(r % N) * ldw + k0 + sq * 8];
+      *(uint4*)&Bs[r][sq * 8] = vb;
+    }
+    __syncthreads();
+    short8 a[4], b[4];
+#pragma unroll
+    for (int mi = 0; mi < 4; mi++)
+      a[mi] = *(const short8*)&As[wm + mi * 16 + l16][quad * 8];
+#pragma unroll
+    for (int ni = 0; ni < 4; ni++)
+      b[ni] = *(const short8*)&Bs[wn + ni * 16 + l16][quad * 8];
+#pragma unroll
+    for (int mi = 0; mi < 4; mi++)
+#pragma unroll
+      for (int ni = 0; ni < 4; ni++)
+        acc[mi][ni] = __builtin_amdgcn_mfma_f32_16x16x32_bf16(
+            a[mi], b[ni], acc[mi][ni], 0, 0, 0);
+    __syncthreads();
+  }
+  float bn[4], wo[4];
+#pragma unroll
+  for (int ni = 0; ni < 4; ni++) {
+    int n = wn + ni * 16 + l16;
+    bn[ni] = bias[n];
+    wo[ni] = wout[n];
+  }
+  float sacc[4][4];
+#pragma unroll
+  for (int mi = 0; mi < 4; mi++)
+#pragma unroll
+    for (int r = 0; r < 4; r++) {
+      float s = 0.f;
+#pragma unroll
+      for (int ni = 0; ni < 4; ni++)
+        s += fmaxf(acc[mi][ni][r] + bn[ni], 0.f) * wo[ni];
+      sacc[mi][r] = s;
+    }
+#pragma unroll
+  for (int off = 1; off < 16; off <<= 1)
+#pragma unroll
+    for (int mi = 0; mi < 4; mi++)
+#pragma unroll
+      for (int r = 0; r < 4; r++)
+        sacc[mi][r] += __shfl_xor(sacc[mi][r], off);
+  int wp = wave & 1;
+  if (l16 == 0) {
+#pragma unroll
+    for (int mi = 0; mi < 4; mi++)
+#pragma unroll
+      for (int r = 0; r < 4; r++)
+        red[wm + mi * 16 + quad * 4 + r][wp] = sacc[mi][r];
+  }
+  __syncthreads();
+  if (tid < 128) {
+    float s = red[tid][0] + red[tid][1] + bout[0];
+    out[(size_t)(m0 + tid)] = 1.f / (1.f + expf(-s));
+  }
+}
+
+__global__ __launch_bounds__(256) void knn_mean4(
+    const float* __restrict__ X,
+    const float* __restrict__ G1,
+    float* __restrict__ X1,
+    __hip_bfloat16* __restrict__ X1b,
+    __hip_bfloat16* __restrict__ X1lo,
+    float* __restrict__ nrmX1)
+{
+  int blk = blockIdx.x;
+  int qb = ((blk & 7) << 11) + ((blk >> 3) << 2);
+  int base = qb & ~2047;
+  int tid = threadIdx.x;
+  int wave = tid >> 6, lane = tid & 63;
+  __shared__ unsigned long long lmins[4][256];
+  __shared__ unsigned long long qmins[4][64];
+  __shared__ unsigned long long thr[4];
+  __shared__ unsigned long long surv[4][256];
+  __shared__ int scnt[4];
+  __shared__ int selidx[4][32];
+  if (tid < 4) scnt[tid] = 0;
+  float xj[8], yj[8];
+#pragma unroll
+  for (int u = 0; u < 8; u++) {
+    int j = (u << 8) + tid;
+    float2 c = *(const float2*)&X[(size_t)(base + j) * 2];
+    xj[u] = c.x;
+    yj[u] = c.y;
+  }
+  unsigned long long key[4][8];
+#pragma unroll
+  for (int g = 0; g < 4; g++) {
+    float qx = X[(size_t)(qb + g) * 2];
+    float qy = X[(size_t)(qb + g) * 2 + 1];
+    unsigned long long lm = ~0ull;
+#pragma unroll
+    for (int u = 0; u < 8; u++) {
+      float dx = xj[u] - qx;
+      float dy = yj[u] - qy;
+      float d2 = dx * dx + dy * dy;
+      key[g][u] = ((unsigned long long)__float_as_uint(d2) << 32) |
+                  (unsigned)((u << 8) + tid);
+      lm = umin64(lm, key[g][u]);
+    }
+    lmins[g][tid] = lm;
+  }
+  __syncthreads();
   {
-    int p = lane;
-    int cnt = (p < c && p < S) ? ((S - 1 - p) / c + 1) : 0;
-    wtab[wave][p] = (float)cnt / (float)S;
-  }
-  const unsigned short* Hs = (const unsigned short*)H;
-  float acc[4] = {0.f, 0.f, 0.f, 0.f};
-  int lim = c < S ? c : S;
-#pragma unroll 4
-  for (int s = 0; s < lim; s++) {
-    float wv = wtab[wave][s];
-    uint2 v = *(const uint2*)&Hs[(size_t)(base + idxl[wave][s]) * CH + lane * 4];
-    acc[0] += wv * __uint_as_float(v.x << 16);
-    acc[1] += wv * __uint_as_float(v.x & 0xffff0000u);
-    acc[2] += wv * __uint_as_float(v.y << 16);
-    acc[3] += wv * __uint_as_float(v.y & 0xffff0000u);
-  }
-  int n0 = lane * 4;
-#pragma unroll
-  for (int j = 0; j < 4; j++)
-    Yb[(size_t)q * ldy + n0 + j] = (__hip_bfloat16)acc[j];
+    int g = wave;
+    unsigned long long qm =
+        umin64(umin64(lmins[g][lane], lmins[g][lane + 64]),
+               umin64(lmins[g][lane + 128], lmins[g][lane + 192]));
+    qmins[g][lane] = qm;
+    int rank = 0;
+    for (int i = 0; i < 64; i++) rank += (qmins[g][i] < qm);
+    if (rank == 31) thr[g] = qm;
+  }
+  __syncthreads();
+#pragma unroll
+  for (int g = 0; g < 4; g++) {
+    unsigned long long T = thr[g];
+#pragma unroll
+    for (int u = 0; u < 8; u++) {
+      if (key[g][u] <= T) {
+        int p = atomicAdd(&scnt[g], 1);
+        if (p < 256) surv[g][p] = key[g][u];
+      }
+    }
+  }
+  __syncthreads();
+  int ovf[4] = {scnt[0], scnt[1], scnt[2], scnt[3]};
+  {
+    int g = wave;
+    int s = ovf[g];
+    if (s <= 256) {
+      for (int i = lane; i < s; i += 64) {
+        unsigned long long c = surv[g][i];
+        int r = 0;
+        for (int j2 = 0; j2 < s; j2++) r += (surv[g][j2] < c);
+        if (r < 32) selidx[g][r] = (int)(c & 0xffffffffULL);
+      }
+    }
+  }
+  if (ovf[0] > 256 || ovf[1] > 256 || ovf[2] > 256 || ovf[3] > 256) {
+    unsigned long long* ob = &lmins[0][0];
+    for (int g = 0; g < 4; g++) {
+      if (ovf[g] <= 256) continue;
+      __syncthreads();
+      if (tid == 0) scnt[g] = 0;
+      __syncthreads();
+      unsigned long long T = thr[g];
+#pragma unroll
+      for (int u = 0; u < 8; u++) {
+        if (key[g][u] <= T) {
+          int p = atomicAdd(&scnt[g], 1);
+          ob[p] = key[g][u];
+        }
+      }
+      __syncthreads();
+      int s2 = scnt[g];
+      for (int i = tid; i < s2; i += 256) {
+        unsigned long long c = ob[i];
+        int r = 0;
+        for (int j2 = 0; j2 < s2; j2++) r += (ob[j2] < c);
+        if (r < 32) selidx[g][r] = (int)(c & 0xffffffffULL);
+      }
+    }
+    __syncthreads();
+  }
+  {
+    int g = wave;
+    float acc = 0.f;
+#pragma unroll 8
+    for (int sI = 0; sI < 32; sI++)
+      acc += G1[(size_t)(base + selidx[g][sI]) * 64 + lane];
+    float v = acc * (1.0f / 32.0f);
+    int q = qb + g;
+    X1[(size_t)q * 64 + lane] = v;
+    __hip_bfloat16 hi = (__hip_bfloat16)v;
+    X1b[(size_t)q * 64 + lane] = hi;
+    X1lo[(size_t)q * 64 + lane] = (__hip_bfloat16)(v - (float)hi);
+    float nv = v * v;
+#pragma unroll
+    for (int off = 32; off > 0; off >>= 1) nv += __shfl_down(nv, off);
+    if (lane == 0) nrmX1[q] = nv;
+  }
 }
 
 extern "C" void kernel_launch(void* const* d_in, const int* in_sizes, int n_in,
@@ -878,8 +886,9 @@
   prologue_kernel<<<off + 256, blk, 0, stream>>>(jb, off, x, sa1_w0, sa1_b0,
                                                  sa1_w1, sa1_b1, G1);
   knn_mean4<<<4096, 256, 0, stream>>>(x, G1, X1, X1b, X1lo, nrmX1);
-  sa2_fused<<<256, blk, 0, stream>>>(X1, sa2_w0, sa2_b0, sa2_w1, sa2_b1, H2);
-  ball_mask_mfma<64><<<dim3(136, 8), blk, 0, stream>>>(X1, X1b, X1lo, nrmX1, MASK, 0.2f * 0.2f);
+  fused_sa2_ball64<<<1088 + 256, blk, 0, stream>>>(
+      X1, X1b, X1lo, nrmX1, MASK, 0.2f * 0.2f,
+      sa2_w0, sa2_b0, sa2_w1, sa2_b1, H2);
   ball_gather4_f32<<<4096, blk, 0, stream>>>(MASK, H2, 128, X2, X2b, X2lo, nrmX2, 128, 32);
   ball_mask_mfma<128><<<dim3(136, 8), blk, 0, stream>>>(X2, X2b, X2lo, nrmX2, MASK, 0.4f * 0.4f);
   {
@@ -897,23 +906,22 @@
       tot1 += g1.xt[i] * 128;
     }
     gemm_mfma_multi<<<tot1, blk, 0, stream>>>(g1);
-
-    GJobs g2;
-    g2.A[0] = (const short*)TB0; g2.W[0] = (const short*)w_sa3_1; g2.bias[0] = sa3_b1;
-    g2.Y[0] = H3b16; g2.lda[0] = 256; g2.ldw[0] = 256; g2.ldy[0] = 256; g2.N[0] = 256; g2.K[0] = 256;
-    g2.A[1] = (const short*)TB1; g2.W[1] = (const short*)w_fp1_1; g2.bias[1] = fp1_b1;
-    g2.Y[1] = G + 256; g2.lda[1] = 512; g2.ldw[1] = 512; g2.ldy[1] = 1024; g2.N[1] = 512; g2.K[1] = 512;
-    g2.A[2] = (const short*)TB2; g2.W[2] = (const short*)w_fp2_1; g2.bias[2] = fp2_b1;
-    g2.Y[2] = G; g2.lda[2] = 256; g2.ldw[2] = 256; g2.ldy[2] = 1024; g2.N[2] = 256; g2.K[2] = 256;
-    int tot2 = 0;
-    for (int i = 0; i < 3; i++) {
-      g2.xt[i] = g2.N[i] >> 7;
-      g2.off[i] = tot2;
-      tot2 += g2.xt[i] * 128;
-    }
-    gemm_mfma_multi<<<tot2, blk, 0, stream>>>(g2);
-  }
-  ball_gather4_bf16<<<4096, blk, 0, stream>>>(MASK, H3b16, 256, G + 768, 1024, 64);
-  gemm_mfma<true><<<dim3(2, 128), blk, 0, stream>>>(G, 1024, w_fc1, 1024, fc1_b, H3b, 256, 256, 1024);
+  }
+  gemm_mfma_bf16<<<dim3(2, 128), blk, 0, stream>>>(TB0, 256, w_sa3_1, 256,
+                                                   sa3_b1, H3b16, 256, 256);
+  {
+    GJobs2 g2;
+    g2.A[0] = (const short*)TB1; g2.W[0] = (const short*)w_fp1_1; g2.bias[0] = fp1_b1;
+    g2.Y[0] = G + 256; g2.lda[0] = 512; g2.ldw[0] = 512; g2.ldy[0] = 1024; g2.K[0] = 512;
+    g2.xt[0] = 4; g2.off[0] = 0;
+    g2.A[1] = (const short*)TB2; g2.W[1] = (const short*)w_fp2_1; g2.bias[1] = fp2_b1;
+    g2.Y[1] = G; g2.lda[1] = 256; g2.ldw[1] = 256; g2.ldy[1] = 1024; g2.K[1] = 256;
+    g2.xt[1] = 2; g2.off[1] = 512;
+    int goff = 768;
+    fused_tail<<<goff + 4096, blk, 0, stream>>>(g2, goff, MASK, H3b16, 256,
+                                                G + 768, 1024, 64);
+  }
+  gemm_mfma_bf16<<<dim3(2, 128), blk, 0, stream>>>(G, 1024, w_fc1, 1024,
+                                                   fc1_b, H3b, 256, 1024);
   gemm_fc2_out<<<dim3(1, 128), blk, 0, stream>>>(H3b, w_fc2, fc2_b, out_w, out_b, out);
 }
```

Result: slower. 364.0 us (+7.0%).
